# Kernel optimization log

Hardware: AMD Instinct MI355X
Metric: run time of the kernel (lower is better)

The kernel has to match this reference:

```python
import jax, jax.numpy as jnp
import numpy as np

QMAX = 7.0            # int4 narrow range: [-7, 7]
SCALING_MIN_VAL = 2e-16


def fake_quant_weight_per_channel(w):
    """Brevitas CommonIntWeightPerChannelQuant, bit_width=4.

    Per-output-channel float scale from abs-max stats, narrow-range signed
    int4 round+clamp, then dequantize. STE so gradients pass through.
    w: [O, I, KH, KW]
    """
    amax = jnp.max(jnp.abs(w), axis=(1, 2, 3), keepdims=True)   # [O,1,1,1]
    scale = jnp.maximum(amax / QMAX, SCALING_MIN_VAL)
    wq = jnp.clip(jnp.round(w / scale), -QMAX, QMAX) * scale
    # straight-through estimator (matches Brevitas round_ste backward)
    return w + jax.lax.stop_gradient(wq - w)


def setup_inputs() -> dict:
    key = jax.random.key(0)
    kx, kw = jax.random.split(key)
    x = jax.random.normal(kx, (32, 256, 56, 56), dtype=jnp.float32)
    # conv weight [out_channels, in_channels, kh, kw]
    w = jax.random.normal(kw, (256, 256, 3, 3), dtype=jnp.float32) * 0.05
    return {"x": x, "w": w}


def reference(x, w):
    wq = fake_quant_weight_per_channel(w)
    return jax.lax.conv_general_dilated(
        x, wq,
        window_strides=(1, 1),
        padding=((1, 1), (1, 1)),
        dimension_numbers=("NCHW", "OIHW", "NCHW"),
    )
```

## Files before the change

### kernel.cpp

```cpp
#include <hip/hip_runtime.h>
#include <cstdint>
#include <cstddef>

typedef __bf16 bf16x8 __attribute__((ext_vector_type(8)));
typedef float  f32x4  __attribute__((ext_vector_type(4)));
typedef int    i32x4  __attribute__((ext_vector_type(4)));

#define QMAX 7.0f
#define SCALE_MIN 2e-16f

#define BAR()     asm volatile("s_barrier" ::: "memory")
#define WAITVM(N) asm volatile("s_waitcnt vmcnt(" #N ")" ::: "memory")

__global__ __launch_bounds__(256) void quant_w_kernel(const float* __restrict__ w,
                                                      __bf16* __restrict__ wq) {
    const int o = blockIdx.x;
    const int t = threadIdx.x;
    const float* wo = w + (size_t)o * 2304;

    float vals[9];
    float m = 0.f;
    #pragma unroll
    for (int i = 0; i < 9; ++i) {
        float v = wo[t + i * 256];
        vals[i] = v;
        m = fmaxf(m, fabsf(v));
    }
    #pragma unroll
    for (int off = 32; off >= 1; off >>= 1) m = fmaxf(m, __shfl_down(m, off));
    __shared__ float red[4];
    __shared__ float s_scale;
    if ((t & 63) == 0) red[t >> 6] = m;
    __syncthreads();
    if (t == 0) {
        float am = fmaxf(fmaxf(red[0], red[1]), fmaxf(red[2], red[3]));
        s_scale = fmaxf(am / QMAX, SCALE_MIN);
    }
    __syncthreads();
    const float scale = s_scale;

    #pragma unroll
    for (int i = 0; i < 9; ++i) {
        int idx = t + i * 256;
        int c = idx / 9;
        int tap = idx - c * 9;
        float q = rintf(vals[i] / scale);
        q = fminf(QMAX, fmaxf(-QMAX, q));
        wq[(size_t)tap * 65536 + (size_t)o * 256 + c] = (__bf16)(q * scale);
    }
}

__global__ __launch_bounds__(256) void convert_x_kernel(const float* __restrict__ x,
                                                        __bf16* __restrict__ xpad) {
    __shared__ float tile[32][33];
    const int n  = blockIdx.z;
    const int c0 = blockIdx.y * 32;
    const int p0 = blockIdx.x * 32;
    const int tx = threadIdx.x & 31;
    const int ty = threadIdx.x >> 5;

    #pragma unroll
    for (int r = 0; r < 4; ++r) {
        int c = c0 + ty + r * 8;
        tile[ty + r * 8][tx] = x[((size_t)(n * 256 + c)) * 3136 + p0 + tx];
    }
    __syncthreads();
    #pragma unroll
    for (int r = 0; r < 4; ++r) {
        int p = p0 + ty + r * 8;
        int h = p / 56, wcol = p - h * 56;
        xpad[(((size_t)n * 58 + h + 1) * 58 + (wcol + 1)) * 256 + c0 + tx] =
            (__bf16)tile[tx][ty + r * 8];
    }
}

__global__ __launch_bounds__(256) void zero_halo_kernel(__bf16* __restrict__ xpad) {
    const int t = blockIdx.x * 256 + threadIdx.x;
    const int cvec = t & 31;
    const int r    = t >> 5;
    const int n    = r / 228;
    const int pos  = r - n * 228;
    if (n >= 32) return;
    int h, wcol;
    if      (pos < 58)  { h = 0;          wcol = pos; }
    else if (pos < 116) { h = 57;         wcol = pos - 58; }
    else if (pos < 172) { h = pos - 115;  wcol = 0; }
    else                { h = pos - 171;  wcol = 57; }
    i32x4* dst = (i32x4*)(xpad + (((size_t)n * 58 + h) * 58 + wcol) * 256);
    dst[cvec] = (i32x4){0, 0, 0, 0};
}

__device__ __forceinline__ void gload_lds16(const void* g, void* l) {
    __builtin_amdgcn_global_load_lds((const __attribute__((address_space(1))) void*)g,
                                     (__attribute__((address_space(3))) void*)l,
                                     16, 0, 0);
}

__global__ __launch_bounds__(256, 2) void conv_mfma_kernel(const __bf16* __restrict__ xpad,
                                                           const __bf16* __restrict__ wq,
                                                           float* __restrict__ out) {
    extern __shared__ __align__(16) char lds[];
    const int tid  = threadIdx.x;
    const int wv   = tid >> 6;
    const int lane = tid & 63;
    const int bid  = blockIdx.x;
    const int swz  = (bid & 7) * 98 + (bid >> 3);
    const int p0   = swz * 128;

    const int wm = wv >> 1;
    const int wn = wv & 1;

    const int trow   = tid >> 2;
    const int schunk = (tid & 3) ^ ((tid >> 5) & 3);
    const __bf16* pA[4];
    #pragma unroll
    for (int j = 0; j < 4; ++j)
        pA[j] = wq + (size_t)(j * 64 + trow) * 256 + schunk * 8;
    const __bf16* pBs[2];
    #pragma unroll
    for (int j = 0; j < 2; ++j) {
        int pos = p0 + j * 64 + trow;
        int ni = pos / 3136;
        int hw = pos - ni * 3136;
        int h = hw / 56, w = hw - h * 56;
        pBs[j] = xpad + (((size_t)ni * 58 + h) * 58 + w) * 256 + schunk * 8;
    }
    const int adst = wv * 1024;
    const int bdst = 16384 + wv * 1024;

    const int l15 = lane & 15;
    const int aoff0 = l15 * 64 + (((lane >> 4) ^ ((lane >> 3) & 1)) << 4);
    const int abase = wm * 8192;
    const int bbase = 16384 + wn * 4096;

    f32x4 acc[8][4];
    #pragma unroll
    for (int m = 0; m < 8; ++m)
        #pragma unroll
        for (int n = 0; n < 4; ++n)
            acc[m][n] = (f32x4){0.f, 0.f, 0.f, 0.f};

    #define STAGE(STEP, BUF)                                                  \
        {                                                                     \
            const int tap_ = (STEP) >> 3, cc_ = (STEP) & 7;                   \
            const int kh_ = tap_ / 3, kw_ = tap_ - kh_ * 3;                   \
            const size_t aoff_ = (size_t)tap_ * 65536 + cc_ * 32;             \
            const size_t boff_ = (size_t)(kh_ * 58 + kw_) * 256 + cc_ * 32;   \
            gload_lds16(pA[0] + aoff_, (BUF) + adst);                         \
            gload_lds16(pA[1] + aoff_, (BUF) + adst + 4096);                  \
            gload_lds16(pA[2] + aoff_, (BUF) + adst + 8192);                  \
            gload_lds16(pA[3] + aoff_, (BUF) + adst + 12288);                 \
            gload_lds16(pBs[0] + boff_, (BUF) + bdst);                        \
            gload_lds16(pBs[1] + boff_, (BUF) + bdst + 4096);                 \
        }

    STAGE(0, lds);

    int co = 0;
    #pragma unroll 1
    for (int s = 0; s < 72; ++s) {
        int no = co + 24576; if (no == 73728) no = 0;
        if (s < 71) {
            STAGE(s + 1, lds + no);
            WAITVM(6);
        } else {
            WAITVM(0);
        }
        BAR();
        const char* B = lds + co;

        bf16x8 a[4], b[4];
        #pragma unroll
        for (int m = 0; m < 4; ++m)
            a[m] = *(const bf16x8*)(B + abase + m * 1024 + (aoff0 ^ ((m & 1) << 5)));
        #pragma unroll
        for (int n = 0; n < 4; ++n)
            b[n] = *(const bf16x8*)(B + bbase + n * 1024 + (aoff0 ^ ((n & 1) << 5)));
        __builtin_amdgcn_s_setprio(1);
        #pragma unroll
        for (int m = 0; m < 4; ++m)
            #pragma unroll
            for (int n = 0; n < 4; ++n)
                acc[m][n] = __builtin_amdgcn_mfma_f32_16x16x32_bf16(a[m], b[n], acc[m][n], 0, 0, 0);
        __builtin_amdgcn_s_setprio(0);
        #pragma unroll
        for (int m = 0; m < 4; ++m)
            a[m] = *(const bf16x8*)(B + abase + (m + 4) * 1024 + (aoff0 ^ ((m & 1) << 5)));
        __builtin_amdgcn_s_setprio(1);
        #pragma unroll
        for (int m = 0; m < 4; ++m)
            #pragma unroll
            for (int n = 0; n < 4; ++n)
                acc[m + 4][n] = __builtin_amdgcn_mfma_f32_16x16x32_bf16(a[m], b[n], acc[m + 4][n], 0, 0, 0);
        __builtin_amdgcn_s_setprio(0);
        co = no;
    }
    #undef STAGE

    #pragma unroll
    for (int n = 0; n < 4; ++n) {
        const int pos = p0 + wn * 64 + n * 16 + l15;
        const int ni = pos / 3136;
        const int hw = pos - ni * 3136;
        float* ob = out + (size_t)ni * 802816 + hw;
        #pragma unroll
        for (int m = 0; m < 8; ++m) {
            const int om = wm * 128 + m * 16 + (lane >> 4) * 4;
            #pragma unroll
            for (int r = 0; r < 4; ++r)
                ob[(size_t)(om + r) * 3136] = acc[m][n][r];
        }
    }
}

__global__ __launch_bounds__(256) void conv_naive_kernel(const float* __restrict__ x,
                                                         const float* __restrict__ w,
                                                         float* __restrict__ out) {
    const int n = blockIdx.z;
    const int o = blockIdx.y;
    const int strip = blockIdx.x;
    __shared__ float wqs[2304];
    __shared__ float red[4];
    __shared__ float s_scale;
    const float* wo = w + (size_t)o * 2304;
    float m = 0.f;
    for (int i = threadIdx.x; i < 2304; i += 256) m = fmaxf(m, fabsf(wo[i]));
    #pragma unroll
    for (int off = 32; off >= 1; off >>= 1) m = fmaxf(m, __shfl_down(m, off));
    if ((threadIdx.x & 63) == 0) red[threadIdx.x >> 6] = m;
    __syncthreads();
    if (threadIdx.x == 0) {
        float am = fmaxf(fmaxf(red[0], red[1]), fmaxf(red[2], red[3]));
        s_scale = fmaxf(am / QMAX, SCALE_MIN);
    }
    __syncthreads();
    const float scale = s_scale;
    for (int i = threadIdx.x; i < 2304; i += 256) {
        float q = rintf(wo[i] / scale);
        q = fminf(QMAX, fmaxf(-QMAX, q));
        wqs[i] = q * scale;
    }
    __syncthreads();
    int p = strip * 256 + threadIdx.x;
    if (p >= 3136) return;
    int h = p / 56, wcol = p - h * 56;
    float acc = 0.f;
    for (int c = 0; c < 256; ++c) {
        const float* xc = x + ((size_t)(n * 256 + c)) * 3136;
        const float* wk = wqs + c * 9;
        #pragma unroll
        for (int kh = 0; kh < 3; ++kh) {
            int hh = h + kh - 1;
            if (hh < 0 || hh > 55) continue;
            #pragma unroll
            for (int kw = 0; kw < 3; ++kw) {
                int ww2 = wcol + kw - 1;
                if (ww2 < 0 || ww2 > 55) continue;
                acc += xc[hh * 56 + ww2] * wk[kh * 3 + kw];
            }
        }
    }
    out[((size_t)(n * 256 + o)) * 3136 + p] = acc;
}

extern "C" void kernel_launch(void* const* d_in, const int* in_sizes, int n_in,
                              void* d_out, int out_size, void* d_ws, size_t ws_size,
                              hipStream_t stream) {
    const float* x = (const float*)d_in[0];
    const float* w = (const float*)d_in[1];
    float* out = (float*)d_out;

    const size_t WQ_BYTES   = 9ull * 256 * 256 * 2;
    const size_t XPAD_OFF   = WQ_BYTES;
    const size_t XPAD_BYTES = 32ull * 58 * 58 * 256 * 2;

    if (ws_size >= XPAD_OFF + XPAD_BYTES) {
        __bf16* wq   = (__bf16*)d_ws;
        __bf16* xpad = (__bf16*)((char*)d_ws + XPAD_OFF);
        hipFuncSetAttribute((const void*)conv_mfma_kernel,
                            hipFuncAttributeMaxDynamicSharedMemorySize, 73728);
        zero_halo_kernel<<<912, 256, 0, stream>>>(xpad);
        quant_w_kernel<<<256, 256, 0, stream>>>(w, wq);
        convert_x_kernel<<<dim3(98, 8, 32), 256, 0, stream>>>(x, xpad);
        conv_mfma_kernel<<<784, 256, 73728, stream>>>(xpad, wq, out);
    } else {
        conv_naive_kernel<<<dim3(13, 256, 32), 256, 0, stream>>>(x, w, out);
    }
}
```

Baseline: 167.8 us.

## Switch conv GEMM to 32x32x16 MFMA with two-stage-ahead prefetch

Replaces the 16x16x32 bf16 MFMA tiling with 32x32x16 MFMA, reorganizing accumulators into 4x2 f32x16 tiles and changing LDS read addressing and the XOR swizzle to match the new fragment layout. The prefetch now keeps two stages in flight, issuing the load for step s+2 after the barrier across the triple buffer. The aim is fewer LDS reads per FLOP, higher MFMA throughput and better hiding of global load latency. It depends on the new swizzle avoiding bank conflicts and on the reordered barrier placement staying race-free.

```diff
diff --git a/kernel.cpp b/kernel.cpp
--- a/kernel.cpp
+++ b/kernel.cpp
@@ -3,7 +3,7 @@
 #include <cstddef>
 
 typedef __bf16 bf16x8 __attribute__((ext_vector_type(8)));
-typedef float  f32x4  __attribute__((ext_vector_type(4)));
+typedef float  f32x16 __attribute__((ext_vector_type(16)));
 typedef int    i32x4  __attribute__((ext_vector_type(4)));
 
 #define QMAX 7.0f
@@ -111,7 +111,7 @@
     const int wn = wv & 1;
 
     const int trow   = tid >> 2;
-    const int schunk = (tid & 3) ^ ((tid >> 5) & 3);
+    const int schunk = (tid & 3) ^ ((tid >> 4) & 3);
     const __bf16* pA[4];
     #pragma unroll
     for (int j = 0; j < 4; ++j)
@@ -128,17 +128,25 @@
     const int adst = wv * 1024;
     const int bdst = 16384 + wv * 1024;
 
-    const int l15 = lane & 15;
-    const int aoff0 = l15 * 64 + (((lane >> 4) ^ ((lane >> 3) & 1)) << 4);
-    const int abase = wm * 8192;
-    const int bbase = 16384 + wn * 4096;
-
-    f32x4 acc[8][4];
-    #pragma unroll
-    for (int m = 0; m < 8; ++m)
-        #pragma unroll
-        for (int n = 0; n < 4; ++n)
-            acc[m][n] = (f32x4){0.f, 0.f, 0.f, 0.f};
+    const int l31 = lane & 31;
+    const int lk  = lane >> 5;
+    const int rsw = (lane >> 2) & 3;
+    int kx[2];
+    #pragma unroll
+    for (int ks = 0; ks < 2; ++ks)
+        kx[ks] = ((ks * 2 + lk) ^ rsw) * 16;
+    int arow[4], brow[2];
+    #pragma unroll
+    for (int m = 0; m < 4; ++m) arow[m] = (wm * 128 + m * 32 + l31) * 64;
+    #pragma unroll
+    for (int n = 0; n < 2; ++n) brow[n] = 16384 + (wn * 64 + n * 32 + l31) * 64;
+
+    f32x16 acc[4][2];
+    #pragma unroll
+    for (int m = 0; m < 4; ++m)
+        #pragma unroll
+        for (int n = 0; n < 2; ++n)
+            acc[m][n] = (f32x16)(0.f);
 
     #define STAGE(STEP, BUF)                                                  \
         {                                                                     \
@@ -155,60 +163,59 @@
         }
 
     STAGE(0, lds);
+    STAGE(1, lds + 24576);
 
     int co = 0;
     #pragma unroll 1
     for (int s = 0; s < 72; ++s) {
-        int no = co + 24576; if (no == 73728) no = 0;
-        if (s < 71) {
-            STAGE(s + 1, lds + no);
-            WAITVM(6);
-        } else {
-            WAITVM(0);
-        }
+        if (s < 71) { WAITVM(6); } else { WAITVM(0); }
         BAR();
+        int so = co + 49152; if (so >= 73728) so -= 73728;
+        if (s < 70) STAGE(s + 2, lds + so);
+
         const char* B = lds + co;
-
-        bf16x8 a[4], b[4];
+        bf16x8 a[4][2], b[2][2];
         #pragma unroll
         for (int m = 0; m < 4; ++m)
-            a[m] = *(const bf16x8*)(B + abase + m * 1024 + (aoff0 ^ ((m & 1) << 5)));
-        #pragma unroll
-        for (int n = 0; n < 4; ++n)
-            b[n] = *(const bf16x8*)(B + bbase + n * 1024 + (aoff0 ^ ((n & 1) << 5)));
+            #pragma unroll
+            for (int ks = 0; ks < 2; ++ks)
+                a[m][ks] = *(const bf16x8*)(B + arow[m] + kx[ks]);
+        #pragma unroll
+        for (int n = 0; n < 2; ++n)
+            #pragma unroll
+            for (int ks = 0; ks < 2; ++ks)
+                b[n][ks] = *(const bf16x8*)(B + brow[n] + kx[ks]);
+
         __builtin_amdgcn_s_setprio(1);
         #pragma unroll
-        for (int m = 0; m < 4; ++m)
-            #pragma unroll
-            for (int n = 0; n < 4; ++n)
-                acc[m][n] = __builtin_amdgcn_mfma_f32_16x16x32_bf16(a[m], b[n], acc[m][n], 0, 0, 0);
+        for (int ks = 0; ks < 2; ++ks)
+            #pragma unroll
+            for (int m = 0; m < 4; ++m)
+                #pragma unroll
+                for (int n = 0; n < 2; ++n)
+                    acc[m][n] = __builtin_amdgcn_mfma_f32_32x32x16_bf16(
+                        a[m][ks], b[n][ks], acc[m][n], 0, 0, 0);
         __builtin_amdgcn_s_setprio(0);
-        #pragma unroll
-        for (int m = 0; m < 4; ++m)
-            a[m] = *(const bf16x8*)(B + abase + (m + 4) * 1024 + (aoff0 ^ ((m & 1) << 5)));
-        __builtin_amdgcn_s_setprio(1);
-        #pragma unroll
-        for (int m = 0; m < 4; ++m)
-            #pragma unroll
-            for (int n = 0; n < 4; ++n)
-                acc[m + 4][n] = __builtin_amdgcn_mfma_f32_16x16x32_bf16(a[m], b[n], acc[m + 4][n], 0, 0, 0);
-        __builtin_amdgcn_s_setprio(0);
-        co = no;
+
+        co += 24576; if (co == 73728) co = 0;
     }
     #undef STAGE
 
-    #pragma unroll
-    for (int n = 0; n < 4; ++n) {
-        const int pos = p0 + wn * 64 + n * 16 + l15;
+    const int hi = lane >> 5;
+    #pragma unroll
+    for (int n = 0; n < 2; ++n) {
+        const int pos = p0 + wn * 64 + n * 32 + l31;
         const int ni = pos / 3136;
         const int hw = pos - ni * 3136;
         float* ob = out + (size_t)ni * 802816 + hw;
         #pragma unroll
-        for (int m = 0; m < 8; ++m) {
-            const int om = wm * 128 + m * 16 + (lane >> 4) * 4;
-            #pragma unroll
-            for (int r = 0; r < 4; ++r)
-                ob[(size_t)(om + r) * 3136] = acc[m][n][r];
+        for (int m = 0; m < 4; ++m) {
+            const int om = wm * 128 + m * 32 + 4 * hi;
+            #pragma unroll
+            for (int r = 0; r < 16; ++r) {
+                const int o = om + (r & 3) + 8 * (r >> 2);
+                ob[(size_t)o * 3136] = acc[m][n][r];
+            }
         }
     }
 }
```

Result: slower. 181.9 us (+8.5%).

## Switch conv GEMM to 256x256 tiles with 8-wave ping-pong interleaved schedule

Applied to the files above, without the earlier changes.

Doubles the block tile to 256 output channels by 256 positions with 512 threads (8 waves) and a 64-wide K step. Global-to-LDS loads are split into small chunks interleaved between MFMA clusters across two LDS buffers, with barriers and lgkmcnt waits sequencing the phases. LDS swizzling changes to a new 128-byte row layout. The aim is higher arithmetic intensity per LDS byte and better overlap of loads with compute. In exchange, the many barriers add sync overhead, and 128 KB of LDS per block limits residency to one block per CU.

```diff
diff --git a/kernel.cpp b/kernel.cpp
--- a/kernel.cpp
+++ b/kernel.cpp
@@ -11,6 +11,8 @@
 
 #define BAR()     asm volatile("s_barrier" ::: "memory")
 #define WAITVM(N) asm volatile("s_waitcnt vmcnt(" #N ")" ::: "memory")
+#define LGKM0()   do { asm volatile("s_waitcnt lgkmcnt(0)" ::: "memory"); \
+                       __builtin_amdgcn_sched_barrier(0); } while (0)
 
 __global__ __launch_bounds__(256) void quant_w_kernel(const float* __restrict__ w,
                                                       __bf16* __restrict__ wq) {
@@ -96,42 +98,46 @@
                                      16, 0, 0);
 }
 
-__global__ __launch_bounds__(256, 2) void conv_mfma_kernel(const __bf16* __restrict__ xpad,
+__global__ __launch_bounds__(512, 2) void conv_mfma_kernel(const __bf16* __restrict__ xpad,
                                                            const __bf16* __restrict__ wq,
                                                            float* __restrict__ out) {
     extern __shared__ __align__(16) char lds[];
     const int tid  = threadIdx.x;
     const int wv   = tid >> 6;
     const int lane = tid & 63;
+    const int l15  = lane & 15;
     const int bid  = blockIdx.x;
-    const int swz  = (bid & 7) * 98 + (bid >> 3);
-    const int p0   = swz * 128;
-
-    const int wm = wv >> 1;
-    const int wn = wv & 1;
-
-    const int trow   = tid >> 2;
-    const int schunk = (tid & 3) ^ ((tid >> 5) & 3);
+    const int swz  = (bid & 7) * 49 + (bid >> 3);
+    const int p0   = swz * 256;
+
+    const int wm = wv >> 2;
+    const int wn = wv & 3;
+
+    const int srow = tid >> 3;
+    const int sks  = ((tid >> 2) ^ (tid >> 3)) & 1;
+    const int slch = (tid & 3) ^ ((tid >> 4) & 3);
+    const int soffk = sks * 32 + slch * 8;
     const __bf16* pA[4];
     #pragma unroll
     for (int j = 0; j < 4; ++j)
-        pA[j] = wq + (size_t)(j * 64 + trow) * 256 + schunk * 8;
-    const __bf16* pBs[2];
-    #pragma unroll
-    for (int j = 0; j < 2; ++j) {
-        int pos = p0 + j * 64 + trow;
+        pA[j] = wq + (size_t)(j * 64 + srow) * 256 + soffk;
+    const __bf16* pB[4];
+    #pragma unroll
+    for (int j = 0; j < 4; ++j) {
+        int pos = p0 + j * 64 + srow;
         int ni = pos / 3136;
         int hw = pos - ni * 3136;
         int h = hw / 56, w = hw - h * 56;
-        pBs[j] = xpad + (((size_t)ni * 58 + h) * 58 + w) * 256 + schunk * 8;
-    }
-    const int adst = wv * 1024;
-    const int bdst = 16384 + wv * 1024;
-
-    const int l15 = lane & 15;
-    const int aoff0 = l15 * 64 + (((lane >> 4) ^ ((lane >> 3) & 1)) << 4);
-    const int abase = wm * 8192;
-    const int bbase = 16384 + wn * 4096;
+        pB[j] = xpad + (((size_t)ni * 58 + h) * 58 + w) * 256 + soffk;
+    }
+    const int wdst = wv * 1024;
+
+    const int swzc = ((lane >> 4) ^ ((l15 >> 1) & 3)) * 16;
+    const int aRd0 = (wm * 128 + l15) * 128 + swzc;
+    const int bRd0 = 32768 + (wn * 64 + l15) * 128 + swzc;
+    int kx[2];
+    kx[0] = (l15 & 1) * 64;
+    kx[1] = (1 - (l15 & 1)) * 64;
 
     f32x4 acc[8][4];
     #pragma unroll
@@ -140,62 +146,147 @@
         for (int n = 0; n < 4; ++n)
             acc[m][n] = (f32x4){0.f, 0.f, 0.f, 0.f};
 
-    #define STAGE(STEP, BUF)                                                  \
-        {                                                                     \
-            const int tap_ = (STEP) >> 3, cc_ = (STEP) & 7;                   \
-            const int kh_ = tap_ / 3, kw_ = tap_ - kh_ * 3;                   \
-            const size_t aoff_ = (size_t)tap_ * 65536 + cc_ * 32;             \
-            const size_t boff_ = (size_t)(kh_ * 58 + kw_) * 256 + cc_ * 32;   \
-            gload_lds16(pA[0] + aoff_, (BUF) + adst);                         \
-            gload_lds16(pA[1] + aoff_, (BUF) + adst + 4096);                  \
-            gload_lds16(pA[2] + aoff_, (BUF) + adst + 8192);                  \
-            gload_lds16(pA[3] + aoff_, (BUF) + adst + 12288);                 \
-            gload_lds16(pBs[0] + boff_, (BUF) + bdst);                        \
-            gload_lds16(pBs[1] + boff_, (BUF) + bdst + 4096);                 \
-        }
-
-    STAGE(0, lds);
-
-    int co = 0;
+    char* const b0 = lds;
+    char* const b1 = lds + 65536;
+
+    #define STG_A(KT, J, BUF)                                                   \
+        gload_lds16(pA[J] + ((size_t)((KT) >> 2) * 65536 + ((KT) & 3) * 64),    \
+                    (BUF) + (J) * 8192 + wdst)
+    #define STG_B(KT, J, BUF)                                                   \
+        gload_lds16(pB[J] + ((size_t)((((KT) >> 2) / 3) * 58 + (((KT) >> 2) % 3)) * 256 \
+                            + ((KT) & 3) * 64),                                 \
+                    (BUF) + 32768 + (J) * 8192 + wdst)
+
+    STG_B(0, 0, b0); STG_B(0, 1, b0); STG_B(0, 2, b0); STG_B(0, 3, b0);
+    STG_A(0, 0, b0); STG_A(0, 1, b0); STG_A(0, 2, b0); STG_A(0, 3, b0);
+    STG_B(1, 0, b1); STG_B(1, 1, b1); STG_B(1, 2, b1); STG_B(1, 3, b1);
+    STG_A(1, 0, b1); STG_A(1, 1, b1);
+    WAITVM(6);
+    BAR();
+
+    bf16x8 a[8], b[4][2];
+
     #pragma unroll 1
-    for (int s = 0; s < 72; ++s) {
-        int no = co + 24576; if (no == 73728) no = 0;
-        if (s < 71) {
-            STAGE(s + 1, lds + no);
-            WAITVM(6);
-        } else {
-            WAITVM(0);
-        }
-        BAR();
-        const char* B = lds + co;
-
-        bf16x8 a[4], b[4];
-        #pragma unroll
-        for (int m = 0; m < 4; ++m)
-            a[m] = *(const bf16x8*)(B + abase + m * 1024 + (aoff0 ^ ((m & 1) << 5)));
-        #pragma unroll
-        for (int n = 0; n < 4; ++n)
-            b[n] = *(const bf16x8*)(B + bbase + n * 1024 + (aoff0 ^ ((n & 1) << 5)));
-        __builtin_amdgcn_s_setprio(1);
-        #pragma unroll
-        for (int m = 0; m < 4; ++m)
-            #pragma unroll
-            for (int n = 0; n < 4; ++n)
-                acc[m][n] = __builtin_amdgcn_mfma_f32_16x16x32_bf16(a[m], b[n], acc[m][n], 0, 0, 0);
-        __builtin_amdgcn_s_setprio(0);
-        #pragma unroll
-        for (int m = 0; m < 4; ++m)
-            a[m] = *(const bf16x8*)(B + abase + (m + 4) * 1024 + (aoff0 ^ ((m & 1) << 5)));
-        __builtin_amdgcn_s_setprio(1);
-        #pragma unroll
-        for (int m = 0; m < 4; ++m)
-            #pragma unroll
-            for (int n = 0; n < 4; ++n)
-                acc[m + 4][n] = __builtin_amdgcn_mfma_f32_16x16x32_bf16(a[m], b[n], acc[m + 4][n], 0, 0, 0);
-        __builtin_amdgcn_s_setprio(0);
-        co = no;
-    }
-    #undef STAGE
+    for (int i = 0; i < 18; ++i) {
+        const int T = 2 * i;
+        const bool g2 = (T + 2 < 36);
+        const bool g3 = (T + 3 < 36);
+        const bool lastw = (i == 17);
+
+        #pragma unroll
+        for (int m = 0; m < 8; ++m)
+            a[m] = *(const bf16x8*)(b0 + aRd0 + m * 2048 + kx[0]);
+        #pragma unroll
+        for (int n = 0; n < 4; ++n) {
+            b[n][0] = *(const bf16x8*)(b0 + bRd0 + n * 2048 + kx[0]);
+            b[n][1] = *(const bf16x8*)(b0 + bRd0 + n * 2048 + kx[1]);
+        }
+        STG_A(T + 1, 2, b1); STG_A(T + 1, 3, b1);
+        BAR(); LGKM0();
+        __builtin_amdgcn_s_setprio(1);
+        #pragma unroll
+        for (int m = 0; m < 8; ++m) {
+            acc[m][0] = __builtin_amdgcn_mfma_f32_16x16x32_bf16(a[m], b[0][0], acc[m][0], 0, 0, 0);
+            acc[m][1] = __builtin_amdgcn_mfma_f32_16x16x32_bf16(a[m], b[1][0], acc[m][1], 0, 0, 0);
+        }
+        __builtin_amdgcn_s_setprio(0);
+        BAR();
+
+        if (g2) { STG_B(T + 2, 0, b0); STG_B(T + 2, 1, b0); }
+        BAR();
+        __builtin_amdgcn_s_setprio(1);
+        #pragma unroll
+        for (int m = 0; m < 8; ++m) {
+            acc[m][2] = __builtin_amdgcn_mfma_f32_16x16x32_bf16(a[m], b[2][0], acc[m][2], 0, 0, 0);
+            acc[m][3] = __builtin_amdgcn_mfma_f32_16x16x32_bf16(a[m], b[3][0], acc[m][3], 0, 0, 0);
+        }
+        __builtin_amdgcn_s_setprio(0);
+        BAR();
+
+        #pragma unroll
+        for (int m = 0; m < 8; ++m)
+            a[m] = *(const bf16x8*)(b0 + aRd0 + m * 2048 + kx[1]);
+        if (g2) { STG_B(T + 2, 2, b0); STG_B(T + 2, 3, b0); }
+        BAR(); LGKM0();
+        __builtin_amdgcn_s_setprio(1);
+        #pragma unroll
+        for (int m = 0; m < 8; ++m) {
+            acc[m][0] = __builtin_amdgcn_mfma_f32_16x16x32_bf16(a[m], b[0][1], acc[m][0], 0, 0, 0);
+            acc[m][1] = __builtin_amdgcn_mfma_f32_16x16x32_bf16(a[m], b[1][1], acc[m][1], 0, 0, 0);
+        }
+        __builtin_amdgcn_s_setprio(0);
+        BAR();
+
+        if (g2) { STG_A(T + 2, 0, b0); STG_A(T + 2, 1, b0); }
+        if (!lastw) { WAITVM(6); } else { WAITVM(0); }
+        BAR();
+        __builtin_amdgcn_s_setprio(1);
+        #pragma unroll
+        for (int m = 0; m < 8; ++m) {
+            acc[m][2] = __builtin_amdgcn_mfma_f32_16x16x32_bf16(a[m], b[2][1], acc[m][2], 0, 0, 0);
+            acc[m][3] = __builtin_amdgcn_mfma_f32_16x16x32_bf16(a[m], b[3][1], acc[m][3], 0, 0, 0);
+        }
+        __builtin_amdgcn_s_setprio(0);
+        BAR();
+
+        #pragma unroll
+        for (int m = 0; m < 8; ++m)
+            a[m] = *(const bf16x8*)(b1 + aRd0 + m * 2048 + kx[0]);
+        #pragma unroll
+        for (int n = 0; n < 4; ++n) {
+            b[n][0] = *(const bf16x8*)(b1 + bRd0 + n * 2048 + kx[0]);
+            b[n][1] = *(const bf16x8*)(b1 + bRd0 + n * 2048 + kx[1]);
+        }
+        if (g2) { STG_A(T + 2, 2, b0); STG_A(T + 2, 3, b0); }
+        BAR(); LGKM0();
+        __builtin_amdgcn_s_setprio(1);
+        #pragma unroll
+        for (int m = 0; m < 8; ++m) {
+            acc[m][0] = __builtin_amdgcn_mfma_f32_16x16x32_bf16(a[m], b[0][0], acc[m][0], 0, 0, 0);
+            acc[m][1] = __builtin_amdgcn_mfma_f32_16x16x32_bf16(a[m], b[1][0], acc[m][1], 0, 0, 0);
+        }
+        __builtin_amdgcn_s_setprio(0);
+        BAR();
+
+        if (g3) { STG_B(T + 3, 0, b1); STG_B(T + 3, 1, b1); }
+        BAR();
+        __builtin_amdgcn_s_setprio(1);
+        #pragma unroll
+        for (int m = 0; m < 8; ++m) {
+            acc[m][2] = __builtin_amdgcn_mfma_f32_16x16x32_bf16(a[m], b[2][0], acc[m][2], 0, 0, 0);
+            acc[m][3] = __builtin_amdgcn_mfma_f32_16x16x32_bf16(a[m], b[3][0], acc[m][3], 0, 0, 0);
+        }
+        __builtin_amdgcn_s_setprio(0);
+        BAR();
+
+        #pragma unroll
+        for (int m = 0; m < 8; ++m)
+            a[m] = *(const bf16x8*)(b1 + aRd0 + m * 2048 + kx[1]);
+        if (g3) { STG_B(T + 3, 2, b1); STG_B(T + 3, 3, b1); }
+        BAR(); LGKM0();
+        __builtin_amdgcn_s_setprio(1);
+        #pragma unroll
+        for (int m = 0; m < 8; ++m) {
+            acc[m][0] = __builtin_amdgcn_mfma_f32_16x16x32_bf16(a[m], b[0][1], acc[m][0], 0, 0, 0);
+            acc[m][1] = __builtin_amdgcn_mfma_f32_16x16x32_bf16(a[m], b[1][1], acc[m][1], 0, 0, 0);
+        }
+        __builtin_amdgcn_s_setprio(0);
+        BAR();
+
+        if (g3) { STG_A(T + 3, 0, b1); STG_A(T + 3, 1, b1); }
+        if (!lastw) { WAITVM(6); } else { WAITVM(0); }
+        BAR();
+        __builtin_amdgcn_s_setprio(1);
+        #pragma unroll
+        for (int m = 0; m < 8; ++m) {
+            acc[m][2] = __builtin_amdgcn_mfma_f32_16x16x32_bf16(a[m], b[2][1], acc[m][2], 0, 0, 0);
+            acc[m][3] = __builtin_amdgcn_mfma_f32_16x16x32_bf16(a[m], b[3][1], acc[m][3], 0, 0, 0);
+        }
+        __builtin_amdgcn_s_setprio(0);
+        BAR();
+    }
+    #undef STG_A
+    #undef STG_B
 
     #pragma unroll
     for (int n = 0; n < 4; ++n) {
@@ -278,11 +369,11 @@
         __bf16* wq   = (__bf16*)d_ws;
         __bf16* xpad = (__bf16*)((char*)d_ws + XPAD_OFF);
         hipFuncSetAttribute((const void*)conv_mfma_kernel,
-                            hipFuncAttributeMaxDynamicSharedMemorySize, 73728);
+                            hipFuncAttributeMaxDynamicSharedMemorySize, 131072);
         zero_halo_kernel<<<912, 256, 0, stream>>>(xpad);
         quant_w_kernel<<<256, 256, 0, stream>>>(w, wq);
         convert_x_kernel<<<dim3(98, 8, 32), 256, 0, stream>>>(x, xpad);
-        conv_mfma_kernel<<<784, 256, 73728, stream>>>(xpad, wq, out);
+        conv_mfma_kernel<<<392, 512, 131072, stream>>>(xpad, wq, out);
     } else {
         conv_naive_kernel<<<dim3(13, 256, 32), 256, 0, stream>>>(x, w, out);
     }
```

Result: slower. 280.2 us (+67.0%).

## Make conv kernel persistent with atomic tile tickets and change LDS swizzle

Applied to the files above, without the earlier changes.

Turns the MFMA conv kernel into a persistent kernel: 512 blocks repeatedly grab 128-position tiles from a global atomic counter that is reset with a memset before launch. Tiles are now visited in linear order instead of the earlier bid swizzle. The LDS XOR swizzle is also changed, on both the store chunk and the read offsets, to cut bank conflicts. The aim is to remove tail imbalance from 784 blocks spread over the CUs. In exchange it adds a memset, an atomic and two barriers per tile, and loses the old L2-locality swizzle.

```diff
diff --git a/kernel.cpp b/kernel.cpp
--- a/kernel.cpp
+++ b/kernel.cpp
@@ -98,117 +98,126 @@
 
 __global__ __launch_bounds__(256, 2) void conv_mfma_kernel(const __bf16* __restrict__ xpad,
                                                            const __bf16* __restrict__ wq,
-                                                           float* __restrict__ out) {
+                                                           float* __restrict__ out,
+                                                           int* __restrict__ ticket) {
     extern __shared__ __align__(16) char lds[];
+    int* s_t = (int*)(lds + 73728);
     const int tid  = threadIdx.x;
     const int wv   = tid >> 6;
     const int lane = tid & 63;
-    const int bid  = blockIdx.x;
-    const int swz  = (bid & 7) * 98 + (bid >> 3);
-    const int p0   = swz * 128;
+    const int l15  = lane & 15;
 
     const int wm = wv >> 1;
     const int wn = wv & 1;
 
     const int trow   = tid >> 2;
-    const int schunk = (tid & 3) ^ ((tid >> 5) & 3);
+    const int schunk = (tid & 3) ^ ((tid >> 3) & 3);
     const __bf16* pA[4];
     #pragma unroll
     for (int j = 0; j < 4; ++j)
         pA[j] = wq + (size_t)(j * 64 + trow) * 256 + schunk * 8;
-    const __bf16* pBs[2];
-    #pragma unroll
-    for (int j = 0; j < 2; ++j) {
-        int pos = p0 + j * 64 + trow;
-        int ni = pos / 3136;
-        int hw = pos - ni * 3136;
-        int h = hw / 56, w = hw - h * 56;
-        pBs[j] = xpad + (((size_t)ni * 58 + h) * 58 + w) * 256 + schunk * 8;
-    }
     const int adst = wv * 1024;
     const int bdst = 16384 + wv * 1024;
 
-    const int l15 = lane & 15;
-    const int aoff0 = l15 * 64 + (((lane >> 4) ^ ((lane >> 3) & 1)) << 4);
+    const int aoff0 = l15 * 64 + ((((lane >> 4) ^ ((l15 >> 1) & 3))) << 4);
     const int abase = wm * 8192;
     const int bbase = 16384 + wn * 4096;
 
-    f32x4 acc[8][4];
-    #pragma unroll
-    for (int m = 0; m < 8; ++m)
+    for (;;) {
+        __syncthreads();
+        if (tid == 0) *s_t = atomicAdd(ticket, 1);
+        __syncthreads();
+        const int tile = *s_t;
+        if (tile >= 784) break;
+        const int p0 = tile * 128;
+
+        const __bf16* pBs[2];
         #pragma unroll
-        for (int n = 0; n < 4; ++n)
-            acc[m][n] = (f32x4){0.f, 0.f, 0.f, 0.f};
-
-    #define STAGE(STEP, BUF)                                                  \
-        {                                                                     \
-            const int tap_ = (STEP) >> 3, cc_ = (STEP) & 7;                   \
-            const int kh_ = tap_ / 3, kw_ = tap_ - kh_ * 3;                   \
-            const size_t aoff_ = (size_t)tap_ * 65536 + cc_ * 32;             \
-            const size_t boff_ = (size_t)(kh_ * 58 + kw_) * 256 + cc_ * 32;   \
-            gload_lds16(pA[0] + aoff_, (BUF) + adst);                         \
-            gload_lds16(pA[1] + aoff_, (BUF) + adst + 4096);                  \
-            gload_lds16(pA[2] + aoff_, (BUF) + adst + 8192);                  \
-            gload_lds16(pA[3] + aoff_, (BUF) + adst + 12288);                 \
-            gload_lds16(pBs[0] + boff_, (BUF) + bdst);                        \
-            gload_lds16(pBs[1] + boff_, (BUF) + bdst + 4096);                 \
+        for (int j = 0; j < 2; ++j) {
+            int pos = p0 + j * 64 + trow;
+            int ni = pos / 3136;
+            int hw = pos - ni * 3136;
+            int h = hw / 56, w = hw - h * 56;
+            pBs[j] = xpad + (((size_t)ni * 58 + h) * 58 + w) * 256 + schunk * 8;
         }
 
-    STAGE(0, lds);
-
-    int co = 0;
-    #pragma unroll 1
-    for (int s = 0; s < 72; ++s) {
-        int no = co + 24576; if (no == 73728) no = 0;
-        if (s < 71) {
-            STAGE(s + 1, lds + no);
-            WAITVM(6);
-        } else {
-            WAITVM(0);
+        f32x4 acc[8][4];
+        #pragma unroll
+        for (int m = 0; m < 8; ++m)
+            #pragma unroll
+            for (int n = 0; n < 4; ++n)
+                acc[m][n] = (f32x4){0.f, 0.f, 0.f, 0.f};
+
+        #define STAGE(STEP, BUF)                                                  \
+            {                                                                     \
+                const int tap_ = (STEP) >> 3, cc_ = (STEP) & 7;                   \
+                const int kh_ = tap_ / 3, kw_ = tap_ - kh_ * 3;                   \
+                const size_t aoff_ = (size_t)tap_ * 65536 + cc_ * 32;             \
+                const size_t boff_ = (size_t)(kh_ * 58 + kw_) * 256 + cc_ * 32;   \
+                gload_lds16(pA[0] + aoff_, (BUF) + adst);                         \
+                gload_lds16(pA[1] + aoff_, (BUF) + adst + 4096);                  \
+                gload_lds16(pA[2] + aoff_, (BUF) + adst + 8192);                  \
+                gload_lds16(pA[3] + aoff_, (BUF) + adst + 12288);                 \
+                gload_lds16(pBs[0] + boff_, (BUF) + bdst);                        \
+                gload_lds16(pBs[1] + boff_, (BUF) + bdst + 4096);                 \
+            }
+
+        STAGE(0, lds);
+
+        int co = 0;
+        #pragma unroll 1
+        for (int s = 0; s < 72; ++s) {
+            int no = co + 24576; if (no == 73728) no = 0;
+            if (s < 71) {
+                STAGE(s + 1, lds + no);
+                WAITVM(6);
+            } else {
+                WAITVM(0);
+            }
+            BAR();
+            const char* B = lds + co;
+
+            bf16x8 a[4], b[4];
+            #pragma unroll
+            for (int m = 0; m < 4; ++m)
+                a[m] = *(const bf16x8*)(B + abase + m * 1024 + aoff0);
+            #pragma unroll
+            for (int n = 0; n < 4; ++n)
+                b[n] = *(const bf16x8*)(B + bbase + n * 1024 + aoff0);
+            __builtin_amdgcn_s_setprio(1);
+            #pragma unroll
+            for (int m = 0; m < 4; ++m)
+                #pragma unroll
+                for (int n = 0; n < 4; ++n)
+                    acc[m][n] = __builtin_amdgcn_mfma_f32_16x16x32_bf16(a[m], b[n], acc[m][n], 0, 0, 0);
+            __builtin_amdgcn_s_setprio(0);
+            #pragma unroll
+            for (int m = 0; m < 4; ++m)
+                a[m] = *(const bf16x8*)(B + abase + (m + 4) * 1024 + aoff0);
+            __builtin_amdgcn_s_setprio(1);
+            #pragma unroll
+            for (int m = 0; m < 4; ++m)
+                #pragma unroll
+                for (int n = 0; n < 4; ++n)
+                    acc[m + 4][n] = __builtin_amdgcn_mfma_f32_16x16x32_bf16(a[m], b[n], acc[m + 4][n], 0, 0, 0);
+            __builtin_amdgcn_s_setprio(0);
+            co = no;
         }
-        BAR();
-        const char* B = lds + co;
-
-        bf16x8 a[4], b[4];
+        #undef STAGE
+
         #pragma unroll
-        for (int m = 0; m < 4; ++m)
-            a[m] = *(const bf16x8*)(B + abase + m * 1024 + (aoff0 ^ ((m & 1) << 5)));
-        #pragma unroll
-        for (int n = 0; n < 4; ++n)
-            b[n] = *(const bf16x8*)(B + bbase + n * 1024 + (aoff0 ^ ((n & 1) << 5)));
-        __builtin_amdgcn_s_setprio(1);
-        #pragma unroll
-        for (int m = 0; m < 4; ++m)
-            #pragma unroll
-            for (int n = 0; n < 4; ++n)
-                acc[m][n] = __builtin_amdgcn_mfma_f32_16x16x32_bf16(a[m], b[n], acc[m][n], 0, 0, 0);
-        __builtin_amdgcn_s_setprio(0);
-        #pragma unroll
-        for (int m = 0; m < 4; ++m)
-            a[m] = *(const bf16x8*)(B + abase + (m + 4) * 1024 + (aoff0 ^ ((m & 1) << 5)));
-        __builtin_amdgcn_s_setprio(1);
-        #pragma unroll
-        for (int m = 0; m < 4; ++m)
-            #pragma unroll
-            for (int n = 0; n < 4; ++n)
-                acc[m + 4][n] = __builtin_amdgcn_mfma_f32_16x16x32_bf16(a[m], b[n], acc[m + 4][n], 0, 0, 0);
-        __builtin_amdgcn_s_setprio(0);
-        co = no;
-    }
-    #undef STAGE
-
-    #pragma unroll
-    for (int n = 0; n < 4; ++n) {
-        const int pos = p0 + wn * 64 + n * 16 + l15;
-        const int ni = pos / 3136;
-        const int hw = pos - ni * 3136;
-        float* ob = out + (size_t)ni * 802816 + hw;
-        #pragma unroll
-        for (int m = 0; m < 8; ++m) {
-            const int om = wm * 128 + m * 16 + (lane >> 4) * 4;
-            #pragma unroll
-            for (int r = 0; r < 4; ++r)
-                ob[(size_t)(om + r) * 3136] = acc[m][n][r];
+        for (int n = 0; n < 4; ++n) {
+            const int pos = p0 + wn * 64 + n * 16 + l15;
+            const int ni = pos / 3136;
+            const int hw = pos - ni * 3136;
+            float* ob = out + (size_t)ni * 802816 + hw;
+            #pragma unroll
+            for (int m = 0; m < 8; ++m) {
+                const int om = wm * 128 + m * 16 + (lane >> 4) * 4;
+                #pragma unroll
+                for (int r = 0; r < 4; ++r)
+                    ob[(size_t)(om + r) * 3136] = acc[m][n][r];
+            }
         }
     }
 }
@@ -273,16 +282,19 @@
     const size_t WQ_BYTES   = 9ull * 256 * 256 * 2;
     const size_t XPAD_OFF   = WQ_BYTES;
     const size_t XPAD_BYTES = 32ull * 58 * 58 * 256 * 2;
-
-    if (ws_size >= XPAD_OFF + XPAD_BYTES) {
+    const size_t TICKET_OFF = XPAD_OFF + XPAD_BYTES;
+
+    if (ws_size >= TICKET_OFF + 64) {
         __bf16* wq   = (__bf16*)d_ws;
         __bf16* xpad = (__bf16*)((char*)d_ws + XPAD_OFF);
+        int* ticket  = (int*)((char*)d_ws + TICKET_OFF);
         hipFuncSetAttribute((const void*)conv_mfma_kernel,
-                            hipFuncAttributeMaxDynamicSharedMemorySize, 73728);
+                            hipFuncAttributeMaxDynamicSharedMemorySize, 73792);
+        hipMemsetAsync(ticket, 0, 4, stream);
         zero_halo_kernel<<<912, 256, 0, stream>>>(xpad);
         quant_w_kernel<<<256, 256, 0, stream>>>(w, wq);
         convert_x_kernel<<<dim3(98, 8, 32), 256, 0, stream>>>(x, xpad);
-        conv_mfma_kernel<<<784, 256, 73728, stream>>>(xpad, wq, out);
+        conv_mfma_kernel<<<512, 256, 73792, stream>>>(xpad, wq, out, ticket);
     } else {
         conv_naive_kernel<<<dim3(13, 256, 32), 256, 0, stream>>>(x, w, out);
     }
```

Result: slower. 175.8 us (+4.8%).
